# Optimization experiments

Measured on AMD Instinct MI355X. Metric: run time of the kernel, lower is better.

The kernel has to match this reference:

```python
import jax, jax.numpy as jnp
import numpy as np

B, N, K = 2, 2048, 32
V = E = H = 128
L = 3
SCALE = 60.0
RS = 0.7071
EPS = 1e-6


def setup_inputs() -> dict:
    key = jax.random.key(0)
    ks = jax.random.split(key, 12)
    C_in = 2 * V + E  # MLP input: [h_V_i, h_V_j(gathered), h_E_ij]
    s = 0.05
    inp = {
        "h_V": jax.random.normal(ks[0], (B, N, V), jnp.float32),
        "h_E": jax.random.normal(ks[1], (B, N, K, E), jnp.float32),
        "topology": jax.random.randint(ks[2], (B, N, K), 0, N),
        "node_w1": jax.random.normal(ks[3], (L, C_in, H), jnp.float32) * s,
        "node_b1": jnp.zeros((L, H), jnp.float32),
        "node_w2": jax.random.normal(ks[4], (L, H, H), jnp.float32) * s,
        "node_b2": jnp.zeros((L, H), jnp.float32),
        "node_w3": jax.random.normal(ks[5], (L, H, V), jnp.float32) * s,
        "node_b3": jnp.zeros((L, V), jnp.float32),
        "ff_w1": jax.random.normal(ks[6], (L, V, H), jnp.float32) * s,
        "ff_b1": jnp.zeros((L, H), jnp.float32),
        "ff_w2": jax.random.normal(ks[7], (L, H, V), jnp.float32) * s,
        "ff_b2": jnp.zeros((L, V), jnp.float32),
        "edge_w1": jax.random.normal(ks[8], (L, C_in, H), jnp.float32) * s,
        "edge_b1": jnp.zeros((L, H), jnp.float32),
        "edge_w2": jax.random.normal(ks[9], (L, H, H), jnp.float32) * s,
        "edge_b2": jnp.zeros((L, H), jnp.float32),
        "edge_w3": jax.random.normal(ks[10], (L, H, E), jnp.float32) * s,
        "edge_b3": jnp.zeros((L, E), jnp.float32),
        "ln1_s": jnp.ones((L, V), jnp.float32), "ln1_b": jnp.zeros((L, V), jnp.float32),
        "ln2_s": jnp.ones((L, V), jnp.float32), "ln2_b": jnp.zeros((L, V), jnp.float32),
        "ln3_s": jnp.ones((L, E), jnp.float32), "ln3_b": jnp.zeros((L, E), jnp.float32),
    }
    return inp


def _ln(x, s, b):
    mu = jnp.mean(x, axis=-1, keepdims=True)
    var = jnp.mean(jnp.square(x - mu), axis=-1, keepdims=True)
    return (x - mu) * jax.lax.rsqrt(var + EPS) * s + b


def _mlp3(x, w1, b1, w2, b2, w3, b3):
    h = jax.nn.gelu(x @ w1 + b1)
    h = jax.nn.gelu(h @ w2 + b2)
    return h @ w3 + b3


def _gather_nodes(h_V, topology):
    # h_V: [B,N,V], topology: [B,N,K] int -> [B,N,K,V]
    return jax.vmap(lambda hv, t: hv[t])(h_V, topology)


def _forward(h_V, h_E, topology, params):
    def step(carry, p):
        h_V, h_E = carry
        (nw1, nb1, nw2, nb2, nw3, nb3, fw1, fb1, fw2, fb2,
         ew1, eb1, ew2, eb2, ew3, eb3, l1s, l1b, l2s, l2b, l3s, l3b) = p
        Bn, Nn, Kn, _ = h_E.shape
        h_Vb = jnp.broadcast_to(h_V[:, :, None, :], (Bn, Nn, Kn, h_V.shape[-1]))
        # [h_V_i, h_V_j, h_E_ij] -> [B,N,K,2V+E]
        h_EV = jnp.concatenate([h_Vb, _gather_nodes(h_V, topology), h_E], axis=-1)
        dh = jnp.sum(_mlp3(h_EV, nw1, nb1, nw2, nb2, nw3, nb3), axis=-2) / SCALE
        h_V = _ln(RS * h_V + dh, l1s, l1b)
        dh = jax.nn.gelu(h_V @ fw1 + fb1) @ fw2 + fb2  # PositionWiseFeedForward
        h_V = _ln(RS * h_V + dh, l2s, l2b)
        h_Vb = jnp.broadcast_to(h_V[:, :, None, :], (Bn, Nn, Kn, h_V.shape[-1]))
        h_EV = jnp.concatenate([h_Vb, _gather_nodes(h_V, topology), h_E], axis=-1)
        h_upd = _mlp3(h_EV, ew1, eb1, ew2, eb2, ew3, eb3)
        h_E = _ln(RS * h_E + h_upd, l3s, l3b)
        return (h_V, h_E), None
    (h_V, h_E), _ = jax.lax.scan(step, (h_V, h_E), params)
    return h_V, h_E


def reference(h_V, h_E, topology, node_w1, node_b1, node_w2, node_b2, node_w3, node_b3,
              ff_w1, ff_b1, ff_w2, ff_b2, edge_w1, edge_b1, edge_w2, edge_b2, edge_w3, edge_b3,
              ln1_s, ln1_b, ln2_s, ln2_b, ln3_s, ln3_b):
    params = (node_w1, node_b1, node_w2, node_b2, node_w3, node_b3,
              ff_w1, ff_b1, ff_w2, ff_b2,
              edge_w1, edge_b1, edge_w2, edge_b2, edge_w3, edge_b3,
              ln1_s, ln1_b, ln2_s, ln2_b, ln3_s, ln3_b)
    return _forward(h_V, h_E, topology, params)
```

## Files before the change

kernel.cpp:

```cpp
#include <hip/hip_runtime.h>
#include <hip/hip_bf16.h>

#define NNODES 4096
#define MEDGES 131072
#define RS 0.7071f

typedef __bf16 bf16x8 __attribute__((ext_vector_type(8)));
typedef float  f32x4  __attribute__((ext_vector_type(4)));

__device__ __forceinline__ float gelu_t(float x){
    const float k0 = 0.7978845608028654f;
    return 0.5f * x * (1.0f + tanhf(k0 * (x + 0.044715f * x * x * x)));
}
__device__ __forceinline__ ushort f2bf(float f){
    __hip_bfloat16 b = __float2bfloat16(f);
    return __builtin_bit_cast(ushort, b);
}


__global__ void pack_acts_kernel(const float* __restrict__ hV, const float* __restrict__ hE,
                                 ushort* __restrict__ hVbf, ushort* __restrict__ hEbf){
    const size_t i0 = (size_t)blockIdx.x * 256 + threadIdx.x;
    const size_t stride = (size_t)gridDim.x * 256;
    for (size_t i = i0; i < 16777216ull; i += stride){
        hEbf[i] = f2bf(hE[i]);
        if (i < 524288ull) hVbf[i] = f2bf(hV[i]);
    }
}

__global__ void pack_w_kernel(const float* __restrict__ nw1, const float* __restrict__ nw2,
                              const float* __restrict__ nw3, const float* __restrict__ ew1,
                              const float* __restrict__ ew2, const float* __restrict__ ew3,
                              ushort* __restrict__ Wp){
    const int id = blockIdx.x * 256 + threadIdx.x;
    const int l = id / 131072, r = id % 131072;
    const float* src; int sidx;
    if (r < 32768){ int col = r >> 8, k = r & 255; src = nw1 + l * 49152; sidx = (128 + k) * 128 + col; }
    else if (r < 65536){ int r2 = r - 32768; int col = r2 >> 8, k = r2 & 255; src = ew1 + l * 49152; sidx = (128 + k) * 128 + col; }
    else {
        int r3 = r - 65536; int m = r3 >> 14; int r4 = r3 & 16383;
        int col = r4 >> 7, k = r4 & 127;
        const float* W = (m == 0) ? nw2 : (m == 1) ? nw3 : (m == 2) ? ew2 : ew3;
        src = W + l * 16384; sidx = k * 128 + col;
    }
    Wp[id] = f2bf(src[sidx]);
}


__device__ __forceinline__ float bsum128(float v, float* red){
    #pragma unroll
    for (int o = 32; o >= 1; o >>= 1) v += __shfl_xor(v, o);
    __syncthreads();
    if ((threadIdx.x & 63) == 0) red[threadIdx.x >> 6] = v;
    __syncthreads();
    return red[0] + red[1];
}

__global__ void __launch_bounds__(128)
b1n0_kernel(const float* __restrict__ hVf, const float* __restrict__ nw1,
            const float* __restrict__ nb1, float* __restrict__ b1n){
    __shared__ float HN[8][132];
    const int u = threadIdx.x;
    const size_t n0 = (size_t)blockIdx.x * 8;
    #pragma unroll
    for (int n = 0; n < 8; ++n) HN[n][u] = hVf[(n0 + n) * 128 + u];
    __syncthreads();
    float a[8];
    #pragma unroll
    for (int n = 0; n < 8; ++n) a[n] = nb1[u];
    for (int c = 0; c < 128; ++c){
        float w = nw1[c * 128 + u];
        #pragma unroll
        for (int n = 0; n < 8; ++n) a[n] = fmaf(HN[n][c], w, a[n]);
    }
    #pragma unroll
    for (int n = 0; n < 8; ++n) b1n[(n0 + n) * 128 + u] = a[n];
}

__global__ void __launch_bounds__(128)
nu_kernel(const float* __restrict__ hVf, const float* __restrict__ dh,
          const float* __restrict__ l1s, const float* __restrict__ l1b,
          const float* __restrict__ l2s, const float* __restrict__ l2b,
          const float* __restrict__ fw1, const float* __restrict__ fb1,
          const float* __restrict__ fw2, const float* __restrict__ fb2,
          const float* __restrict__ ew1, const float* __restrict__ eb1,
          const float* __restrict__ nw1n, const float* __restrict__ nb1n,
          float* __restrict__ hVf_out, ushort* __restrict__ hVbf,
          float* __restrict__ b1e, float* __restrict__ b1n){
    __shared__ float X1[8][132], G[8][132], HN[8][132];
    __shared__ float red[2];
    const int u = threadIdx.x;
    const size_t n0 = (size_t)blockIdx.x * 8;
    float xv[8], a[8];
    #pragma unroll
    for (int n = 0; n < 8; ++n)
        xv[n] = RS * hVf[(n0 + n) * 128 + u] + dh[(n0 + n) * 128 + u] * (1.f / 60.f);
    #pragma unroll
    for (int n = 0; n < 8; ++n){
        float mu = bsum128(xv[n], red) * (1.f / 128.f);
        float d = xv[n] - mu;
        float var = bsum128(d * d, red) * (1.f / 128.f);
        float y = d * rsqrtf(var + 1e-6f) * l1s[u] + l1b[u];
        X1[n][u] = y; xv[n] = y;
    }
    __syncthreads();
    #pragma unroll
    for (int n = 0; n < 8; ++n) a[n] = fb1[u];
    for (int c = 0; c < 128; ++c){
        float w = fw1[c * 128 + u];
        #pragma unroll
        for (int n = 0; n < 8; ++n) a[n] = fmaf(X1[n][c], w, a[n]);
    }
    #pragma unroll
    for (int n = 0; n < 8; ++n) G[n][u] = gelu_t(a[n]);
    __syncthreads();
    #pragma unroll
    for (int n = 0; n < 8; ++n) a[n] = fb2[u];
    for (int c = 0; c < 128; ++c){
        float w = fw2[c * 128 + u];
        #pragma unroll
        for (int n = 0; n < 8; ++n) a[n] = fmaf(G[n][c], w, a[n]);
    }
    #pragma unroll
    for (int n = 0; n < 8; ++n){
        float x = RS * xv[n] + a[n];
        float mu = bsum128(x, red) * (1.f / 128.f);
        float d = x - mu;
        float var = bsum128(d * d, red) * (1.f / 128.f);
        float hv = d * rsqrtf(var + 1e-6f) * l2s[u] + l2b[u];
        HN[n][u] = hv;
        hVf_out[(n0 + n) * 128 + u] = hv;
        hVbf[(n0 + n) * 128 + u] = f2bf(hv);
    }
    __syncthreads();
    #pragma unroll
    for (int n = 0; n < 8; ++n) a[n] = eb1[u];
    for (int c = 0; c < 128; ++c){
        float w = ew1[c * 128 + u];
        #pragma unroll
        for (int n = 0; n < 8; ++n) a[n] = fmaf(HN[n][c], w, a[n]);
    }
    #pragma unroll
    for (int n = 0; n < 8; ++n) b1e[(n0 + n) * 128 + u] = a[n];
    if (nw1n){
        #pragma unroll
        for (int n = 0; n < 8; ++n) a[n] = nb1n[u];
        for (int c = 0; c < 128; ++c){
            float w = nw1n[c * 128 + u];
            #pragma unroll
            for (int n = 0; n < 8; ++n) a[n] = fmaf(HN[n][c], w, a[n]);
        }
        #pragma unroll
        for (int n = 0; n < 8; ++n) b1n[(n0 + n) * 128 + u] = a[n];
    }
}


template<int NCH, int MODE, bool GATHER>
__global__ void __launch_bounds__(512, 1)
gemm_kernel(const ushort* __restrict__ Asrc, const ushort* __restrict__ hVbf,
            const ushort* __restrict__ hEbf, const int* __restrict__ topo,
            const ushort* __restrict__ Bp, const float* __restrict__ cinit,
            ushort* __restrict__ Hout, float* __restrict__ dh,
            const float* __restrict__ hEf_in, float* __restrict__ hEf_out,
            ushort* __restrict__ hEbf_out,
            const float* __restrict__ lnS, const float* __restrict__ lnB)
{
    __shared__ __align__(16) char smem[71680];
    ushort* Abuf = (ushort*)smem;
    ushort* Bbuf = (ushort*)(smem + 32768);
    int*    sJ   = (int*)(smem + 69632);
    float*  sLn  = (float*)(smem + 70656);

    const int t = threadIdx.x;
    const int lane = t & 63, wave = t >> 6;
    const int wr = wave >> 1, wc = wave & 1;
    const size_t bR = (size_t)blockIdx.x * 256;

    if (GATHER && t < 256){
        int rg = blockIdx.x * 256 + t;
        sJ[t] = topo[rg] + ((rg >> 16) << 11);
    }
    if (MODE == 2 && t < 128){ sLn[t] = lnS[t]; sLn[128 + t] = lnB[t]; }
    __syncthreads();

    f32x4 acc[4][4];
    {
        const int colb = wc * 64 + (lane & 15);
        #pragma unroll
        for (int rt = 0; rt < 4; ++rt){
            float v4[4];
            #pragma unroll
            for (int ct = 0; ct < 4; ++ct){
                int colg = colb + ct * 16;
                float v;
                if (GATHER){
                    int node = blockIdx.x * 8 + wr * 2 + (rt >> 1);
                    v = cinit[(size_t)node * 128 + colg];
                } else v = cinit[colg];
                v4[ct] = v;
            }
            #pragma unroll
            for (int ct = 0; ct < 4; ++ct){
                f32x4 z = {v4[ct], v4[ct], v4[ct], v4[ct]};
                acc[rt][ct] = z;
            }
        }
    }

    uint4 pa[4]; uint4 pb[2];
    const int arow = t >> 1, ah = t & 1;
    const int bcol = t >> 2, bq = t & 3;

    auto loadch = [&](int ch){
        const ushort* s;
        if (GATHER){
            if (ch < 2) s = hVbf + (size_t)sJ[arow] * 128 + (ch & 1) * 64;
            else        s = hEbf + (bR + arow) * 128 + (ch & 1) * 64;
        } else {
            s = Asrc + (bR + arow) * 128 + ch * 64;
        }
        const uint4* s4 = (const uint4*)s;
        #pragma unroll
        for (int i = 0; i < 4; ++i) pa[i] = s4[ah * 4 + i];
        const uint4* b4 = (const uint4*)(Bp + (size_t)bcol * (NCH * 64) + ch * 64);
        #pragma unroll
        for (int i = 0; i < 2; ++i) pb[i] = b4[bq * 2 + i];
    };
    auto writech = [&](){
        #pragma unroll
        for (int i = 0; i < 4; ++i){
            int c = ah * 4 + i;
            *(uint4*)(Abuf + arow * 64 + ((c ^ (arow & 7)) << 3)) = pa[i];
        }
        #pragma unroll
        for (int i = 0; i < 2; ++i){
            int c = bq * 2 + i;
            *(uint4*)(Bbuf + bcol * 64 + ((c ^ (bcol & 7)) << 3)) = pb[i];
        }
    };

    loadch(0); writech(); __syncthreads();

    for (int ch = 0; ch < NCH; ++ch){
        if (ch + 1 < NCH) loadch(ch + 1);
        #pragma unroll
        for (int ks = 0; ks < 2; ++ks){
            bf16x8 af[4], bfr[4];
            const int cc = ks * 4 + (lane >> 4);
            #pragma unroll
            for (int rt = 0; rt < 4; ++rt){
                int row = wr * 64 + rt * 16 + (lane & 15);
                af[rt] = *(const bf16x8*)(Abuf + row * 64 + ((cc ^ (row & 7)) << 3));
            }
            #pragma unroll
            for (int ct = 0; ct < 4; ++ct){
                int col = wc * 64 + ct * 16 + (lane & 15);
                bfr[ct] = *(const bf16x8*)(Bbuf + col * 64 + ((cc ^ (col & 7)) << 3));
            }
            #pragma unroll
            for (int rt = 0; rt < 4; ++rt)
                #pragma unroll
                for (int ct = 0; ct < 4; ++ct)
                    acc[rt][ct] = __builtin_amdgcn_mfma_f32_16x16x32_bf16(af[rt], bfr[ct], acc[rt][ct], 0, 0, 0);
        }
        __syncthreads();
        if (ch + 1 < NCH){ writech(); __syncthreads(); }
    }

    if (MODE == 0){
        ushort* Tb = (ushort*)smem;
        #pragma unroll
        for (int rt = 0; rt < 4; ++rt)
            #pragma unroll
            for (int ct = 0; ct < 4; ++ct){
                int col = wc * 64 + ct * 16 + (lane & 15);
                #pragma unroll
                for (int r = 0; r < 4; ++r){
                    int row = wr * 64 + rt * 16 + ((lane >> 4) << 2) + r;
                    Tb[row * 136 + col] = f2bf(gelu_t(acc[rt][ct][r]));
                }
            }
        __syncthreads();
        const int row = t >> 1;
        #pragma unroll
        for (int i = 0; i < 8; ++i){
            int c16 = (t & 1) + 2 * i;
            uint4 v = *(const uint4*)(Tb + row * 136 + c16 * 8);
            *(uint4*)(Hout + (bR + row) * 128 + c16 * 8) = v;
        }
    }

    if (MODE == 1 || MODE == 2){
        float* Tf = (float*)smem;
        #pragma unroll
        for (int p = 0; p < 2; ++p){
            if ((wr >> 1) == p){
                #pragma unroll
                for (int rt = 0; rt < 4; ++rt)
                    #pragma unroll
                    for (int ct = 0; ct < 4; ++ct){
                        int col = wc * 64 + ct * 16 + (lane & 15);
                        #pragma unroll
                        for (int r = 0; r < 4; ++r){
                            int row = (wr & 1) * 64 + rt * 16 + ((lane >> 4) << 2) + r;
                            Tf[row * 132 + col] = acc[rt][ct][r];
                        }
                    }
            }
            __syncthreads();
            if (MODE == 1){
                int col = t & 127, g = t >> 7;
                float s = 0.f;
                #pragma unroll 8
                for (int r = 0; r < 32; ++r) s += Tf[(g * 32 + r) * 132 + col];
                dh[((size_t)blockIdx.x * 8 + p * 4 + g) * 128 + col] = s;
            } else {
                #pragma unroll
                for (int rr = 0; rr < 2; ++rr){
                    int row = (t >> 3) + rr * 64;
                    int j = t & 7;
                    size_t rowg = bR + p * 128 + row;
                    const float* tr = Tf + row * 132 + j * 16;
                    const float* ri = hEf_in + rowg * 128 + j * 16;
                    float x[16]; float s = 0.f;
                    #pragma unroll
                    for (int i = 0; i < 16; ++i){ x[i] = RS * ri[i] + tr[i]; s += x[i]; }
                    s += __shfl_xor(s, 1); s += __shfl_xor(s, 2); s += __shfl_xor(s, 4);
                    float mu = s * (1.f / 128.f);
                    float vv = 0.f;
                    #pragma unroll
                    for (int i = 0; i < 16; ++i){ float d = x[i] - mu; vv += d * d; }
                    vv += __shfl_xor(vv, 1); vv += __shfl_xor(vv, 2); vv += __shfl_xor(vv, 4);
                    float rstd = rsqrtf(vv * (1.f / 128.f) + 1e-6f);
                    float o[16];
                    #pragma unroll
                    for (int i = 0; i < 16; ++i){
                        int col = j * 16 + i;
                        o[i] = (x[i] - mu) * rstd * sLn[col] + sLn[128 + col];
                    }
                    #pragma unroll
                    for (int i = 0; i < 4; ++i)
                        *(float4*)(hEf_out + rowg * 128 + j * 16 + i * 4) =
                            make_float4(o[i * 4], o[i * 4 + 1], o[i * 4 + 2], o[i * 4 + 3]);
                    uint4 u0, u1;
                    u0.x = (uint)f2bf(o[0])  | ((uint)f2bf(o[1])  << 16);
                    u0.y = (uint)f2bf(o[2])  | ((uint)f2bf(o[3])  << 16);
                    u0.z = (uint)f2bf(o[4])  | ((uint)f2bf(o[5])  << 16);
                    u0.w = (uint)f2bf(o[6])  | ((uint)f2bf(o[7])  << 16);
                    u1.x = (uint)f2bf(o[8])  | ((uint)f2bf(o[9])  << 16);
                    u1.y = (uint)f2bf(o[10]) | ((uint)f2bf(o[11]) << 16);
                    u1.z = (uint)f2bf(o[12]) | ((uint)f2bf(o[13]) << 16);
                    u1.w = (uint)f2bf(o[14]) | ((uint)f2bf(o[15]) << 16);
                    *(uint4*)(hEbf_out + rowg * 128 + j * 16)     = u0;
                    *(uint4*)(hEbf_out + rowg * 128 + j * 16 + 8) = u1;
                }
            }
            __syncthreads();
        }
    }
}


extern "C" void kernel_launch(void* const* d_in, const int* in_sizes, int n_in,
                              void* d_out, int out_size, void* d_ws, size_t ws_size,
                              hipStream_t stream)
{
    (void)in_sizes; (void)n_in; (void)out_size; (void)ws_size;

    const float* hV0  = (const float*)d_in[0];
    const float* hE0  = (const float*)d_in[1];
    const int*   topo = (const int*)  d_in[2];
    const float* nw1  = (const float*)d_in[3];
    const float* nb1  = (const float*)d_in[4];
    const float* nw2  = (const float*)d_in[5];
    const float* nb2  = (const float*)d_in[6];
    const float* nw3  = (const float*)d_in[7];
    const float* nb3  = (const float*)d_in[8];
    const float* fw1  = (const float*)d_in[9];
    const float* fb1  = (const float*)d_in[10];
    const float* fw2  = (const float*)d_in[11];
    const float* fb2  = (const float*)d_in[12];
    const float* ew1  = (const float*)d_in[13];
    const float* eb1  = (const float*)d_in[14];
    const float* ew2  = (const float*)d_in[15];
    const float* eb2  = (const float*)d_in[16];
    const float* ew3  = (const float*)d_in[17];
    const float* eb3  = (const float*)d_in[18];
    const float* l1s  = (const float*)d_in[19];
    const float* l1b  = (const float*)d_in[20];
    const float* l2s  = (const float*)d_in[21];
    const float* l2b  = (const float*)d_in[22];
    const float* l3s  = (const float*)d_in[23];
    const float* l3b  = (const float*)d_in[24];

    float* out_hV = (float*)d_out;
    float* out_hE = out_hV + 524288;

    char* ws = (char*)d_ws;
    ushort* Hbf   = (ushort*)(ws);
    ushort* hEbf  = (ushort*)(ws + 33554432);
    ushort* hVbf  = (ushort*)(ws + 67108864);
    float*  hVf1  = (float*) (ws + 68157440);
    float*  hVf2  = (float*) (ws + 70254592);
    float*  b1n   = (float*) (ws + 72351744);
    float*  b1e   = (float*) (ws + 74448896);
    float*  dh    = (float*) (ws + 76546048);
    ushort* Wp    = (ushort*)(ws + 78643200);

    pack_acts_kernel<<<2048, 256, 0, stream>>>(hV0, hE0, hVbf, hEbf);
    pack_w_kernel<<<1536, 256, 0, stream>>>(nw1, nw2, nw3, ew1, ew2, ew3, Wp);
    b1n0_kernel<<<512, 128, 0, stream>>>(hV0, nw1, nb1, b1n);

    for (int l = 0; l < 3; ++l){
        const ushort* p_n1 = Wp + (size_t)l * 131072;
        const ushort* p_e1 = p_n1 + 32768;
        const ushort* p_n2 = p_n1 + 65536;
        const ushort* p_n3 = p_n1 + 81920;
        const ushort* p_e2 = p_n1 + 98304;
        const ushort* p_e3 = p_n1 + 114688;

        const float* hVf_cur = (l == 0) ? hV0 : (l == 1) ? hVf1 : hVf2;
        float*       hVf_nxt = (l == 0) ? hVf1 : (l == 1) ? hVf2 : out_hV;
        const float* hEf_in  = (l == 0) ? hE0 : out_hE;

        gemm_kernel<4,0,true ><<<512, 512, 0, stream>>>(nullptr, hVbf, hEbf, topo, p_n1, b1n,
            Hbf, nullptr, nullptr, nullptr, nullptr, nullptr, nullptr);
        gemm_kernel<2,0,false><<<512, 512, 0, stream>>>(Hbf, nullptr, nullptr, nullptr, p_n2, nb2 + l*128,
            Hbf, nullptr, nullptr, nullptr, nullptr, nullptr, nullptr);
        gemm_kernel<2,1,false><<<512, 512, 0, stream>>>(Hbf, nullptr, nullptr, nullptr, p_n3, nb3 + l*128,
            nullptr, dh, nullptr, nullptr, nullptr, nullptr, nullptr);

        nu_kernel<<<512, 128, 0, stream>>>(hVf_cur, dh,
            l1s + l*128, l1b + l*128, l2s + l*128, l2b + l*128,
            fw1 + l*16384, fb1 + l*128, fw2 + l*16384, fb2 + l*128,
            ew1 + (size_t)l*49152, eb1 + l*128,
            (l < 2) ? nw1 + (size_t)(l+1)*49152 : nullptr,
            (l < 2) ? nb1 + (l+1)*128 : nullptr,
            hVf_nxt, hVbf, b1e, b1n);

        gemm_kernel<4,0,true ><<<512, 512, 0, stream>>>(nullptr, hVbf, hEbf, topo, p_e1, b1e,
            Hbf, nullptr, nullptr, nullptr, nullptr, nullptr, nullptr);
        gemm_kernel<2,0,false><<<512, 512, 0, stream>>>(Hbf, nullptr, nullptr, nullptr, p_e2, eb2 + l*128,
            Hbf, nullptr, nullptr, nullptr, nullptr, nullptr, nullptr);
        gemm_kernel<2,2,false><<<512, 512, 0, stream>>>(Hbf, nullptr, nullptr, nullptr, p_e3, eb3 + l*128,
            nullptr, nullptr, hEf_in, out_hE, hEbf, l3s + l*128, l3b + l*128);
    }
}
```

Measured before the change: 1.062 ms.

## Replace scalar node-update kernel with LN kernel plus bf16 MFMA GEMM launches

Removes the per-node scalar FP32 nu_kernel and b1n0_kernel. Their work is split into a wave-per-row LayerNorm kernel and several launches of the existing bf16 MFMA gemm_kernel, which handles the feed-forward, LN2 and the node-side first-layer projections. pack_w now also packs the FF and the node-part W1 weights, and a new GEMM mode writes plain fp32 output. The goal is to run the small node-level matmuls on matrix cores instead of serial FMA loops. In exchange it adds several extra launches with only 16 blocks each, and moves these projections to bf16 precision.

```diff
diff --git a/kernel.cpp b/kernel.cpp
--- a/kernel.cpp
+++ b/kernel.cpp
@@ -1,8 +1,6 @@
 #include <hip/hip_runtime.h>
 #include <hip/hip_bf16.h>
 
-#define NNODES 4096
-#define MEDGES 131072
 #define RS 0.7071f
 
 typedef __bf16 bf16x8 __attribute__((ext_vector_type(8)));
@@ -31,128 +29,56 @@
 __global__ void pack_w_kernel(const float* __restrict__ nw1, const float* __restrict__ nw2,
                               const float* __restrict__ nw3, const float* __restrict__ ew1,
                               const float* __restrict__ ew2, const float* __restrict__ ew3,
+                              const float* __restrict__ fw1, const float* __restrict__ fw2,
                               ushort* __restrict__ Wp){
     const int id = blockIdx.x * 256 + threadIdx.x;
-    const int l = id / 131072, r = id % 131072;
+    const int l = id / 196608, r = id % 196608;
     const float* src; int sidx;
-    if (r < 32768){ int col = r >> 8, k = r & 255; src = nw1 + l * 49152; sidx = (128 + k) * 128 + col; }
-    else if (r < 65536){ int r2 = r - 32768; int col = r2 >> 8, k = r2 & 255; src = ew1 + l * 49152; sidx = (128 + k) * 128 + col; }
+    if (r < 32768){ int col = r >> 8, k = r & 255; src = nw1 + (size_t)l * 49152; sidx = (128 + k) * 128 + col; }
+    else if (r < 65536){ int r2 = r - 32768; int col = r2 >> 8, k = r2 & 255; src = ew1 + (size_t)l * 49152; sidx = (128 + k) * 128 + col; }
     else {
         int r3 = r - 65536; int m = r3 >> 14; int r4 = r3 & 16383;
         int col = r4 >> 7, k = r4 & 127;
-        const float* W = (m == 0) ? nw2 : (m == 1) ? nw3 : (m == 2) ? ew2 : ew3;
-        src = W + l * 16384; sidx = k * 128 + col;
+        const float* W;
+        switch (m){
+            case 0: W = nw2 + (size_t)l * 16384; break;
+            case 1: W = nw3 + (size_t)l * 16384; break;
+            case 2: W = ew2 + (size_t)l * 16384; break;
+            case 3: W = ew3 + (size_t)l * 16384; break;
+            case 4: W = fw1 + (size_t)l * 16384; break;
+            case 5: W = fw2 + (size_t)l * 16384; break;
+            case 6: W = nw1 + (size_t)l * 49152; break;
+            default:W = ew1 + (size_t)l * 49152; break;
+        }
+        src = W; sidx = k * 128 + col;
     }
     Wp[id] = f2bf(src[sidx]);
 }
 
 
-__device__ __forceinline__ float bsum128(float v, float* red){
+__global__ void __launch_bounds__(256)
+ln1_kernel(const float* __restrict__ hVf, const float* __restrict__ dh,
+           const float* __restrict__ l1s, const float* __restrict__ l1b,
+           float* __restrict__ X1f, ushort* __restrict__ X1bf){
+    const int lane = threadIdx.x & 63, w = threadIdx.x >> 6;
+    const size_t row = (size_t)blockIdx.x * 4 + w;
+    const float2 hv = *(const float2*)(hVf + row * 128 + lane * 2);
+    const float2 dv = *(const float2*)(dh  + row * 128 + lane * 2);
+    float x0 = fmaf(RS, hv.x, dv.x * (1.f / 60.f));
+    float x1 = fmaf(RS, hv.y, dv.y * (1.f / 60.f));
+    float s = x0 + x1;
+    #pragma unroll
+    for (int o = 32; o >= 1; o >>= 1) s += __shfl_xor(s, o);
+    const float mu = s * (1.f / 128.f);
+    const float d0 = x0 - mu, d1 = x1 - mu;
+    float v = d0 * d0 + d1 * d1;
     #pragma unroll
     for (int o = 32; o >= 1; o >>= 1) v += __shfl_xor(v, o);
-    __syncthreads();
-    if ((threadIdx.x & 63) == 0) red[threadIdx.x >> 6] = v;
-    __syncthreads();
-    return red[0] + red[1];
-}
-
-__global__ void __launch_bounds__(128)
-b1n0_kernel(const float* __restrict__ hVf, const float* __restrict__ nw1,
-            const float* __restrict__ nb1, float* __restrict__ b1n){
-    __shared__ float HN[8][132];
-    const int u = threadIdx.x;
-    const size_t n0 = (size_t)blockIdx.x * 8;
-    #pragma unroll
-    for (int n = 0; n < 8; ++n) HN[n][u] = hVf[(n0 + n) * 128 + u];
-    __syncthreads();
-    float a[8];
-    #pragma unroll
-    for (int n = 0; n < 8; ++n) a[n] = nb1[u];
-    for (int c = 0; c < 128; ++c){
-        float w = nw1[c * 128 + u];
-        #pragma unroll
-        for (int n = 0; n < 8; ++n) a[n] = fmaf(HN[n][c], w, a[n]);
-    }
-    #pragma unroll
-    for (int n = 0; n < 8; ++n) b1n[(n0 + n) * 128 + u] = a[n];
-}
-
-__global__ void __launch_bounds__(128)
-nu_kernel(const float* __restrict__ hVf, const float* __restrict__ dh,
-          const float* __restrict__ l1s, const float* __restrict__ l1b,
-          const float* __restrict__ l2s, const float* __restrict__ l2b,
-          const float* __restrict__ fw1, const float* __restrict__ fb1,
-          const float* __restrict__ fw2, const float* __restrict__ fb2,
-          const float* __restrict__ ew1, const float* __restrict__ eb1,
-          const float* __restrict__ nw1n, const float* __restrict__ nb1n,
-          float* __restrict__ hVf_out, ushort* __restrict__ hVbf,
-          float* __restrict__ b1e, float* __restrict__ b1n){
-    __shared__ float X1[8][132], G[8][132], HN[8][132];
-    __shared__ float red[2];
-    const int u = threadIdx.x;
-    const size_t n0 = (size_t)blockIdx.x * 8;
-    float xv[8], a[8];
-    #pragma unroll
-    for (int n = 0; n < 8; ++n)
-        xv[n] = RS * hVf[(n0 + n) * 128 + u] + dh[(n0 + n) * 128 + u] * (1.f / 60.f);
-    #pragma unroll
-    for (int n = 0; n < 8; ++n){
-        float mu = bsum128(xv[n], red) * (1.f / 128.f);
-        float d = xv[n] - mu;
-        float var = bsum128(d * d, red) * (1.f / 128.f);
-        float y = d * rsqrtf(var + 1e-6f) * l1s[u] + l1b[u];
-        X1[n][u] = y; xv[n] = y;
-    }
-    __syncthreads();
-    #pragma unroll
-    for (int n = 0; n < 8; ++n) a[n] = fb1[u];
-    for (int c = 0; c < 128; ++c){
-        float w = fw1[c * 128 + u];
-        #pragma unroll
-        for (int n = 0; n < 8; ++n) a[n] = fmaf(X1[n][c], w, a[n]);
-    }
-    #pragma unroll
-    for (int n = 0; n < 8; ++n) G[n][u] = gelu_t(a[n]);
-    __syncthreads();
-    #pragma unroll
-    for (int n = 0; n < 8; ++n) a[n] = fb2[u];
-    for (int c = 0; c < 128; ++c){
-        float w = fw2[c * 128 + u];
-        #pragma unroll
-        for (int n = 0; n < 8; ++n) a[n] = fmaf(G[n][c], w, a[n]);
-    }
-    #pragma unroll
-    for (int n = 0; n < 8; ++n){
-        float x = RS * xv[n] + a[n];
-        float mu = bsum128(x, red) * (1.f / 128.f);
-        float d = x - mu;
-        float var = bsum128(d * d, red) * (1.f / 128.f);
-        float hv = d * rsqrtf(var + 1e-6f) * l2s[u] + l2b[u];
-        HN[n][u] = hv;
-        hVf_out[(n0 + n) * 128 + u] = hv;
-        hVbf[(n0 + n) * 128 + u] = f2bf(hv);
-    }
-    __syncthreads();
-    #pragma unroll
-    for (int n = 0; n < 8; ++n) a[n] = eb1[u];
-    for (int c = 0; c < 128; ++c){
-        float w = ew1[c * 128 + u];
-        #pragma unroll
-        for (int n = 0; n < 8; ++n) a[n] = fmaf(HN[n][c], w, a[n]);
-    }
-    #pragma unroll
-    for (int n = 0; n < 8; ++n) b1e[(n0 + n) * 128 + u] = a[n];
-    if (nw1n){
-        #pragma unroll
-        for (int n = 0; n < 8; ++n) a[n] = nb1n[u];
-        for (int c = 0; c < 128; ++c){
-            float w = nw1n[c * 128 + u];
-            #pragma unroll
-            for (int n = 0; n < 8; ++n) a[n] = fmaf(HN[n][c], w, a[n]);
-        }
-        #pragma unroll
-        for (int n = 0; n < 8; ++n) b1n[(n0 + n) * 128 + u] = a[n];
-    }
+    const float rstd = rsqrtf(v * (1.f / 128.f) + 1e-6f);
+    const float y0 = d0 * rstd * l1s[lane * 2]     + l1b[lane * 2];
+    const float y1 = d1 * rstd * l1s[lane * 2 + 1] + l1b[lane * 2 + 1];
+    *(float2*)(X1f + row * 128 + lane * 2) = make_float2(y0, y1);
+    ((uint*)X1bf)[row * 64 + lane] = (uint)f2bf(y0) | ((uint)f2bf(y1) << 16);
 }
 
 
@@ -161,9 +87,9 @@
 gemm_kernel(const ushort* __restrict__ Asrc, const ushort* __restrict__ hVbf,
             const ushort* __restrict__ hEbf, const int* __restrict__ topo,
             const ushort* __restrict__ Bp, const float* __restrict__ cinit,
-            ushort* __restrict__ Hout, float* __restrict__ dh,
-            const float* __restrict__ hEf_in, float* __restrict__ hEf_out,
-            ushort* __restrict__ hEbf_out,
+            ushort* __restrict__ Hout, float* __restrict__ fOut,
+            const float* __restrict__ resid_in, float* __restrict__ lnOut,
+            ushort* __restrict__ bfOut,
             const float* __restrict__ lnS, const float* __restrict__ lnB)
 {
     __shared__ __align__(16) char smem[71680];
@@ -189,7 +115,6 @@
         const int colb = wc * 64 + (lane & 15);
         #pragma unroll
         for (int rt = 0; rt < 4; ++rt){
-            float v4[4];
             #pragma unroll
             for (int ct = 0; ct < 4; ++ct){
                 int colg = colb + ct * 16;
@@ -198,11 +123,7 @@
                     int node = blockIdx.x * 8 + wr * 2 + (rt >> 1);
                     v = cinit[(size_t)node * 128 + colg];
                 } else v = cinit[colg];
-                v4[ct] = v;
-            }
-            #pragma unroll
-            for (int ct = 0; ct < 4; ++ct){
-                f32x4 z = {v4[ct], v4[ct], v4[ct], v4[ct]};
+                f32x4 z = {v, v, v, v};
                 acc[rt][ct] = z;
             }
         }
@@ -291,7 +212,7 @@
         }
     }
 
-    if (MODE == 1 || MODE == 2){
+    if (MODE == 1 || MODE == 2 || MODE == 4){
         float* Tf = (float*)smem;
         #pragma unroll
         for (int p = 0; p < 2; ++p){
@@ -314,7 +235,14 @@
                 float s = 0.f;
                 #pragma unroll 8
                 for (int r = 0; r < 32; ++r) s += Tf[(g * 32 + r) * 132 + col];
-                dh[((size_t)blockIdx.x * 8 + p * 4 + g) * 128 + col] = s;
+                fOut[((size_t)blockIdx.x * 8 + p * 4 + g) * 128 + col] = s;
+            } else if (MODE == 4){
+                const int row = t >> 2, q = t & 3;
+                #pragma unroll
+                for (int i = 0; i < 8; ++i){
+                    float4 v = *(const float4*)(Tf + row * 132 + q * 32 + i * 4);
+                    *(float4*)(fOut + (bR + p * 128 + row) * 128 + q * 32 + i * 4) = v;
+                }
             } else {
                 #pragma unroll
                 for (int rr = 0; rr < 2; ++rr){
@@ -322,10 +250,10 @@
                     int j = t & 7;
                     size_t rowg = bR + p * 128 + row;
                     const float* tr = Tf + row * 132 + j * 16;
-                    const float* ri = hEf_in + rowg * 128 + j * 16;
+                    const float* ri = resid_in + rowg * 128 + j * 16;
                     float x[16]; float s = 0.f;
                     #pragma unroll
-                    for (int i = 0; i < 16; ++i){ x[i] = RS * ri[i] + tr[i]; s += x[i]; }
+                    for (int i = 0; i < 16; ++i){ x[i] = fmaf(RS, ri[i], tr[i]); s += x[i]; }
                     s += __shfl_xor(s, 1); s += __shfl_xor(s, 2); s += __shfl_xor(s, 4);
                     float mu = s * (1.f / 128.f);
                     float vv = 0.f;
@@ -341,7 +269,7 @@
                     }
                     #pragma unroll
                     for (int i = 0; i < 4; ++i)
-                        *(float4*)(hEf_out + rowg * 128 + j * 16 + i * 4) =
+                        *(float4*)(lnOut + rowg * 128 + j * 16 + i * 4) =
                             make_float4(o[i * 4], o[i * 4 + 1], o[i * 4 + 2], o[i * 4 + 3]);
                     uint4 u0, u1;
                     u0.x = (uint)f2bf(o[0])  | ((uint)f2bf(o[1])  << 16);
@@ -352,8 +280,8 @@
                     u1.y = (uint)f2bf(o[10]) | ((uint)f2bf(o[11]) << 16);
                     u1.z = (uint)f2bf(o[12]) | ((uint)f2bf(o[13]) << 16);
                     u1.w = (uint)f2bf(o[14]) | ((uint)f2bf(o[15]) << 16);
-                    *(uint4*)(hEbf_out + rowg * 128 + j * 16)     = u0;
-                    *(uint4*)(hEbf_out + rowg * 128 + j * 16 + 8) = u1;
+                    *(uint4*)(bfOut + rowg * 128 + j * 16)     = u0;
+                    *(uint4*)(bfOut + rowg * 128 + j * 16 + 8) = u1;
                 }
             }
             __syncthreads();
@@ -373,19 +301,12 @@
     const int*   topo = (const int*)  d_in[2];
     const float* nw1  = (const float*)d_in[3];
     const float* nb1  = (const float*)d_in[4];
-    const float* nw2  = (const float*)d_in[5];
     const float* nb2  = (const float*)d_in[6];
-    const float* nw3  = (const float*)d_in[7];
     const float* nb3  = (const float*)d_in[8];
-    const float* fw1  = (const float*)d_in[9];
     const float* fb1  = (const float*)d_in[10];
-    const float* fw2  = (const float*)d_in[11];
     const float* fb2  = (const float*)d_in[12];
-    const float* ew1  = (const float*)d_in[13];
     const float* eb1  = (const float*)d_in[14];
-    const float* ew2  = (const float*)d_in[15];
     const float* eb2  = (const float*)d_in[16];
-    const float* ew3  = (const float*)d_in[17];
     const float* eb3  = (const float*)d_in[18];
     const float* l1s  = (const float*)d_in[19];
     const float* l1b  = (const float*)d_in[20];
@@ -401,27 +322,36 @@
     ushort* Hbf   = (ushort*)(ws);
     ushort* hEbf  = (ushort*)(ws + 33554432);
     ushort* hVbf  = (ushort*)(ws + 67108864);
-    float*  hVf1  = (float*) (ws + 68157440);
-    float*  hVf2  = (float*) (ws + 70254592);
-    float*  b1n   = (float*) (ws + 72351744);
-    float*  b1e   = (float*) (ws + 74448896);
-    float*  dh    = (float*) (ws + 76546048);
-    ushort* Wp    = (ushort*)(ws + 78643200);
+    float*  b1n   = (float*) (ws + 68157440);
+    float*  b1e   = (float*) (ws + 70254592);
+    float*  dh    = (float*) (ws + 72351744);
+    float*  X1f   = (float*) (ws + 74448896);
+    ushort* X1bf  = (ushort*)(ws + 76546048);
+    ushort* Gbf   = (ushort*)(ws);
+    ushort* Wp    = (ushort*)(ws + 77594624);
 
     pack_acts_kernel<<<2048, 256, 0, stream>>>(hV0, hE0, hVbf, hEbf);
-    pack_w_kernel<<<1536, 256, 0, stream>>>(nw1, nw2, nw3, ew1, ew2, ew3, Wp);
-    b1n0_kernel<<<512, 128, 0, stream>>>(hV0, nw1, nb1, b1n);
+    pack_w_kernel<<<2304, 256, 0, stream>>>(nw1, (const float*)d_in[5], (const float*)d_in[7],
+                                            (const float*)d_in[13], (const float*)d_in[15],
+                                            (const float*)d_in[17], (const float*)d_in[9],
+                                            (const float*)d_in[11], Wp);
+    gemm_kernel<2,4,false><<<16, 512, 0, stream>>>(hVbf, nullptr, nullptr, nullptr,
+        Wp + 163840, nb1, nullptr, b1n, nullptr, nullptr, nullptr, nullptr, nullptr);
 
     for (int l = 0; l < 3; ++l){
-        const ushort* p_n1 = Wp + (size_t)l * 131072;
-        const ushort* p_e1 = p_n1 + 32768;
-        const ushort* p_n2 = p_n1 + 65536;
-        const ushort* p_n3 = p_n1 + 81920;
-        const ushort* p_e2 = p_n1 + 98304;
-        const ushort* p_e3 = p_n1 + 114688;
-
-        const float* hVf_cur = (l == 0) ? hV0 : (l == 1) ? hVf1 : hVf2;
-        float*       hVf_nxt = (l == 0) ? hVf1 : (l == 1) ? hVf2 : out_hV;
+        const ushort* pL   = Wp + (size_t)l * 196608;
+        const ushort* p_n1 = pL;
+        const ushort* p_e1 = pL + 32768;
+        const ushort* p_n2 = pL + 65536;
+        const ushort* p_n3 = pL + 81920;
+        const ushort* p_e2 = pL + 98304;
+        const ushort* p_e3 = pL + 114688;
+        const ushort* p_f1 = pL + 131072;
+        const ushort* p_f2 = pL + 147456;
+        const ushort* p_e1a= pL + 180224;
+
+        const float* hVf_cur = (l == 0) ? hV0 : out_hV;
+        float*       hVf_nxt = out_hV;
         const float* hEf_in  = (l == 0) ? hE0 : out_hE;
 
         gemm_kernel<4,0,true ><<<512, 512, 0, stream>>>(nullptr, hVbf, hEbf, topo, p_n1, b1n,
@@ -431,13 +361,18 @@
         gemm_kernel<2,1,false><<<512, 512, 0, stream>>>(Hbf, nullptr, nullptr, nullptr, p_n3, nb3 + l*128,
             nullptr, dh, nullptr, nullptr, nullptr, nullptr, nullptr);
 
-        nu_kernel<<<512, 128, 0, stream>>>(hVf_cur, dh,
-            l1s + l*128, l1b + l*128, l2s + l*128, l2b + l*128,
-            fw1 + l*16384, fb1 + l*128, fw2 + l*16384, fb2 + l*128,
-            ew1 + (size_t)l*49152, eb1 + l*128,
-            (l < 2) ? nw1 + (size_t)(l+1)*49152 : nullptr,
-            (l < 2) ? nb1 + (l+1)*128 : nullptr,
-            hVf_nxt, hVbf, b1e, b1n);
+        ln1_kernel<<<1024, 256, 0, stream>>>(hVf_cur, dh, l1s + l*128, l1b + l*128, X1f, X1bf);
+        gemm_kernel<2,0,false><<<16, 512, 0, stream>>>(X1bf, nullptr, nullptr, nullptr, p_f1, fb1 + l*128,
+            Gbf, nullptr, nullptr, nullptr, nullptr, nullptr, nullptr);
+        gemm_kernel<2,2,false><<<16, 512, 0, stream>>>(Gbf, nullptr, nullptr, nullptr, p_f2, fb2 + l*128,
+            nullptr, nullptr, X1f, hVf_nxt, hVbf, l2s + l*128, l2b + l*128);
+
+        gemm_kernel<2,4,false><<<16, 512, 0, stream>>>(hVbf, nullptr, nullptr, nullptr, p_e1a, eb1 + l*128,
+            nullptr, b1e, nullptr, nullptr, nullptr, nullptr, nullptr);
+        if (l < 2)
+            gemm_kernel<2,4,false><<<16, 512, 0, stream>>>(hVbf, nullptr, nullptr, nullptr,
+                Wp + (size_t)(l+1) * 196608 + 163840, nb1 + (l+1)*128,
+                nullptr, b1n, nullptr, nullptr, nullptr, nullptr, nullptr);
 
         gemm_kernel<4,0,true ><<<512, 512, 0, stream>>>(nullptr, hVbf, hEbf, topo, p_e1, b1e,
             Hbf, nullptr, nullptr, nullptr, nullptr, nullptr, nullptr);
```

After: 1.044 ms. About the same (-1.7%).
